# Kernel optimization log

Hardware: AMD Instinct MI355X
Metric: run time of the kernel (lower is better)

The kernel has to match this reference:

```python
import jax, jax.numpy as jnp
import numpy as np

K = 4  # knn_graph(k=4, loop=False) hard-coded in H2GCN.forward


def _knn_2hop_adj(Fet, k):
    """Per-batch kNN graph -> symmetrize -> 2-hop binary adjacency [B,N,N].

    Matches create_adj + get_2hop_neighbors: edge direction and the row
    normalization in create_adj are irrelevant because get_2hop_neighbors
    symmetrizes (adj[row,col]=adj[col,row]=1) and thresholds (adj@adj > 0).
    """
    B, N, _ = Fet.shape
    sq = jnp.sum(Fet * Fet, axis=-1)  # [B,N]
    dist = sq[:, :, None] + sq[:, None, :] - 2.0 * jnp.einsum('bnf,bmf->bnm', Fet, Fet)
    eye = jnp.eye(N, dtype=bool)
    dist = jnp.where(eye[None], jnp.inf, dist)  # loop=False: exclude self
    _, idx = jax.lax.top_k(-dist, k)  # [B,N,k] nearest-neighbor indices
    b_idx = jnp.arange(B)[:, None, None]
    n_idx = jnp.arange(N)[None, :, None]
    A = jnp.zeros((B, N, N), Fet.dtype).at[b_idx, n_idx, idx].set(1.0)
    A = jnp.maximum(A, jnp.swapaxes(A, 1, 2))  # symmetrize 1-hop
    A2 = jnp.einsum('bnm,bmk->bnk', A, A)      # 2-hop counts
    A2 = jnp.where(eye[None], 0.0, A2)          # fill_diagonal_(0)
    return (A2 > 0).astype(Fet.dtype)


def _h2gcn_conv(x, A2, w1, b1, w2, b2):
    """H2GCNConv on dense binary adjacency.

    Dense matmul with binary A2 == gather(x[col]) -> fc2 -> index_add over rows;
    A2.sum(-1) == bincount(row). Degree clamped to >= 1.
    """
    ego = jnp.einsum('bnf,of->bno', x, w1) + b1   # fc1(x)
    msg = jnp.einsum('bnf,of->bno', x, w2) + b2   # fc2(x)
    agg = jnp.einsum('bnm,bmo->bno', A2, msg)     # scatter-add of neighbor msgs
    deg = jnp.maximum(jnp.sum(A2, axis=-1, keepdims=True), 1.0)
    return jax.nn.relu(jnp.concatenate([ego, agg / deg], axis=-1))


def setup_inputs() -> dict:
    key = jax.random.key(0)
    ks = jax.random.split(key, 8)
    B, N, F, NH, NC = 128, 197, 768, 512, 1000
    s = 0.02
    return {
        'Fet': jax.random.normal(ks[0], (B, N, F), jnp.float32),
        'w1_0': jax.random.normal(ks[1], (NH, F), jnp.float32) * s,
        'b1_0': jnp.zeros((NH,), jnp.float32),
        'w2_0': jax.random.normal(ks[2], (NH, F), jnp.float32) * s,
        'b2_0': jnp.zeros((NH,), jnp.float32),
        'w1_1': jax.random.normal(ks[3], (NH, 2 * NH), jnp.float32) * s,
        'b1_1': jnp.zeros((NH,), jnp.float32),
        'w2_1': jax.random.normal(ks[4], (NH, 2 * NH), jnp.float32) * s,
        'b2_1': jnp.zeros((NH,), jnp.float32),
        'fc1_w': jax.random.normal(ks[5], (NH, 4 * NH), jnp.float32) * s,
        'fc1_b': jnp.zeros((NH,), jnp.float32),
        'fc2_w': jax.random.normal(ks[6], (NC, NH), jnp.float32) * s,
        'fc2_b': jnp.zeros((NC,), jnp.float32),
    }


def reference(Fet, w1_0, b1_0, w2_0, b2_0, w1_1, b1_1, w2_1, b2_1,
              fc1_w, fc1_b, fc2_w, fc2_b):
    A2 = _knn_2hop_adj(Fet, K)
    h1 = _h2gcn_conv(Fet, A2, w1_0, b1_0, w2_0, b2_0)   # [B,N,2*nhid]
    h2 = _h2gcn_conv(h1, A2, w1_1, b1_1, w2_1, b2_1)    # [B,N,2*nhid]
    h = jnp.concatenate([h1, h2], axis=-1)              # [B,N,final_dim]
    graph_features = jnp.mean(h, axis=1)                # global_mean_pool
    p = jax.nn.relu(graph_features @ fc1_w.T + fc1_b)   # dropout is identity (eval)
    out = p @ fc2_w.T + fc2_b
    return (out, graph_features)
```

## Files before the change

### kernel.cpp

```cpp
#include <hip/hip_runtime.h>
#include <hip/hip_bf16.h>
#include <math.h>

typedef __attribute__((ext_vector_type(8))) short bf16x8;
typedef __attribute__((ext_vector_type(4))) float f32x4;

#define B_ 128
#define N_ 197
#define F_ 768
#define NH_ 512
#define D2_ 1024
#define D4_ 2048
#define NC_ 1000
#define ROWS_ (B_ * N_)
#define KA_ 224
#define NA_ 256
#define LDG_ 200
#define MT_LD_ (B_ * KA_)

#define OFF_G0     0ull
#define OFF_SQ     20172800ull
#define OFF_ABITS  20273664ull
#define OFF_DEG    21080576ull
#define OFF_FETHI  21181440ull
#define OFF_MSGT   60011520ull
#define OFF_H1     89371648ull
#define OFF_FETLO  OFF_MSGT
#define OFF_POOL   141014016ull
#define OFF_P      142062592ull
#define OFF_WC1    142324736ull
#define OFF_WC2    143897600ull
#define OFF_G1     145994752ull

__device__ __forceinline__ void gll16(const void* g, void* l) {
  __builtin_amdgcn_global_load_lds((const __attribute__((address_space(1))) void*)g,
                                   (__attribute__((address_space(3))) void*)l, 16, 0, 0);
}


__global__ __launch_bounds__(256) void cast_weights(const float* __restrict__ w10,
                                                    const float* __restrict__ w20,
                                                    const float* __restrict__ w11,
                                                    const float* __restrict__ w21,
                                                    __hip_bfloat16* __restrict__ wc1,
                                                    __hip_bfloat16* __restrict__ wc2) {
  const int S1 = NH_ * F_ / 4;
  const int S2 = NH_ * D2_ / 4;
  int i = blockIdx.x * 256 + threadIdx.x;
  const float* src;
  __hip_bfloat16* dst;
  int off;
  if (i < S1) { src = w10; dst = wc1; off = i; }
  else if (i < 2 * S1) { src = w20; dst = wc1 + (size_t)NH_ * F_; off = i - S1; }
  else if (i < 2 * S1 + S2) { src = w11; dst = wc2; off = i - 2 * S1; }
  else { src = w21; dst = wc2 + (size_t)NH_ * D2_; off = i - 2 * S1 - S2; }
  float4 v = ((const float4*)src)[off];
  union { __hip_bfloat16 h[4]; uint2 u; } pk;
  pk.h[0] = __float2bfloat16(v.x);
  pk.h[1] = __float2bfloat16(v.y);
  pk.h[2] = __float2bfloat16(v.z);
  pk.h[3] = __float2bfloat16(v.w);
  ((uint2*)dst)[off] = pk.u;
}

__global__ __launch_bounds__(256) void cast_hilo_sq(const float* __restrict__ X,
                                                    __hip_bfloat16* __restrict__ hi,
                                                    __hip_bfloat16* __restrict__ lo,
                                                    float* __restrict__ sq) {
  int row = blockIdx.x * 4 + (threadIdx.x >> 6);
  int lane = threadIdx.x & 63;
  const float4* xp = (const float4*)(X + (size_t)row * F_);
  uint2* hp = (uint2*)(hi + (size_t)row * F_);
  uint2* lp = (uint2*)(lo + (size_t)row * F_);
  float s = 0.f;
#pragma unroll
  for (int i = 0; i < 3; i++) {
    float4 v = xp[lane + i * 64];
    s += v.x * v.x + v.y * v.y + v.z * v.z + v.w * v.w;
    float f[4] = {v.x, v.y, v.z, v.w};
    union { __hip_bfloat16 h[4]; uint2 u; } ph, pl;
#pragma unroll
    for (int k = 0; k < 4; k++) {
      __hip_bfloat16 h = __float2bfloat16(f[k]);
      ph.h[k] = h;
      pl.h[k] = __float2bfloat16(f[k] - __bfloat162float(h));
    }
    hp[lane + i * 64] = ph.u;
    lp[lane + i * 64] = pl.u;
  }
#pragma unroll
  for (int o = 32; o > 0; o >>= 1) s += __shfl_down(s, o);
  if (lane == 0) sq[row] = s;
}

__global__ __launch_bounds__(256) void mfma_gram(const __hip_bfloat16* __restrict__ Xhi,
                                                 const __hip_bfloat16* __restrict__ Xlo,
                                                 float* __restrict__ g0,
                                                 float* __restrict__ g1) {
  __shared__ short AsH[4096];
  __shared__ short BsH[4096];
  __shared__ short AsL[4096];
  __shared__ short BsL[4096];
  const int t = threadIdx.x;
  const int wgid = blockIdx.x;
  const int L = (wgid & 7) * 96 + (wgid >> 3);
  const int b = L / 6;
  const int rbx = L - b * 6;
  const int bx = rbx % 3;
  const int khalf = rbx / 3;
  const int m0 = (bx == 0) ? 0 : 128;
  const int o0 = (bx == 2) ? 128 : 0;
  const bool mirror = (bx == 1);
  const int l = t & 63, w = t >> 6;
  const int wm = (w >> 1) * 64, wn = (w & 1) * 64;
  const int frow = l & 15, fch = l >> 4;
  const size_t rowbase = (size_t)b * N_;
  const char* AhiB = (const char*)(Xhi + (rowbase + m0) * F_);
  const char* AloB = (const char*)(Xlo + (rowbase + m0) * F_);
  const char* BhiB = (const char*)(Xhi + (rowbase + o0) * F_);
  const char* BloB = (const char*)(Xlo + (rowbase + o0) * F_);
  const int rb = F_ * 2;
  char* AsHB = (char*)AsH;
  char* BsHB = (char*)BsH;
  char* AsLB = (char*)AsL;
  char* BsLB = (char*)BsL;
  float* go = khalf ? g1 : g0;
  f32x4 zero = {0.f, 0.f, 0.f, 0.f};
  f32x4 acc[4][4];
#pragma unroll
  for (int i = 0; i < 4; i++)
#pragma unroll
    for (int j = 0; j < 4; j++) acc[i][j] = zero;
  const int kt0 = khalf * 12;
  for (int kt = kt0; kt < kt0 + 12; kt++) {
    const int kb = kt * 64;
#pragma unroll
    for (int u = 0; u < 2; u++) {
      int prow = u * 32 + (t >> 3);
      int e = (t & 7) ^ (prow & 7);
      int grow = (e >> 2) * 64 + prow;
      size_t goff = (size_t)grow * rb + kb + (e & 3) * 16;
      gll16(AhiB + goff, AsHB + u * 4096 + t * 16);
      gll16(BhiB + goff, BsHB + u * 4096 + t * 16);
      gll16(AloB + goff, AsLB + u * 4096 + t * 16);
      gll16(BloB + goff, BsLB + u * 4096 + t * 16);
    }
    __syncthreads();
    bf16x8 ah[4], al[4], bh[4], bl[4];
#pragma unroll
    for (int i = 0; i < 4; i++) {
      int ar = wm + i * 16 + frow;
      int apr = ar & 63;
      int aoff = apr * 128 + (((((ar >> 6) << 2) | fch) ^ (apr & 7)) * 16);
      ah[i] = *(const bf16x8*)(AsHB + aoff);
      al[i] = *(const bf16x8*)(AsLB + aoff);
      int br = wn + i * 16 + frow;
      int bpr = br & 63;
      int boff = bpr * 128 + (((((br >> 6) << 2) | fch) ^ (bpr & 7)) * 16);
      bh[i] = *(const bf16x8*)(BsHB + boff);
      bl[i] = *(const bf16x8*)(BsLB + boff);
    }
#pragma unroll
    for (int i = 0; i < 4; i++)
#pragma unroll
      for (int j = 0; j < 4; j++) {
        acc[i][j] = __builtin_amdgcn_mfma_f32_16x16x32_bf16(bh[j], ah[i], acc[i][j], 0, 0, 0);
        acc[i][j] = __builtin_amdgcn_mfma_f32_16x16x32_bf16(bl[j], ah[i], acc[i][j], 0, 0, 0);
        acc[i][j] = __builtin_amdgcn_mfma_f32_16x16x32_bf16(bh[j], al[i], acc[i][j], 0, 0, 0);
      }
    __syncthreads();
  }
#pragma unroll
  for (int i = 0; i < 4; i++) {
    int n = m0 + wm + i * 16 + frow;
    if (n >= N_) continue;
    float* gr = go + (rowbase + n) * LDG_;
#pragma unroll
    for (int j = 0; j < 4; j++) {
      int mb = o0 + wn + j * 16 + fch * 4;
      if (mb >= LDG_) continue;
      f32x4 pv = acc[i][j];
      *(f32x4*)&gr[mb] = pv;
      if (mirror) {
#pragma unroll
        for (int r = 0; r < 4; r++)
          go[(rowbase + mb + r) * LDG_ + n] = pv[r];
      }
    }
  }
}

__global__ __launch_bounds__(256) void topk_kernel(const float* __restrict__ g0,
                                                   const float* __restrict__ g1,
                                                   const float* __restrict__ sq,
                                                   unsigned long long* __restrict__ Abits) {
  int row = blockIdx.x * 4 + (threadIdx.x >> 6);
  int lane = threadIdx.x & 63;
  int b = row / N_, n = row - b * N_;
  const float* g0r = g0 + (size_t)row * LDG_;
  const float* g1r = g1 + (size_t)row * LDG_;
  const float* sqb = sq + (size_t)b * N_;
  float v[4];
  int vi[4];
#pragma unroll
  for (int i = 0; i < 4; i++) {
    int m = lane + i * 64;
    bool ok = (m < N_) && (m != n);
    v[i] = ok ? (sqb[m] - 2.f * (g0r[m] + g1r[m])) : INFINITY;
    vi[i] = ok ? m : 0x3fffffff;
  }
  unsigned long long nbr[4] = {0ull, 0ull, 0ull, 0ull};
#pragma unroll
  for (int t = 0; t < 4; t++) {
    float bv = v[0];
    int bi = vi[0];
#pragma unroll
    for (int i = 1; i < 4; i++)
      if (v[i] < bv || (v[i] == bv && vi[i] < bi)) { bv = v[i]; bi = vi[i]; }
#pragma unroll
    for (int o = 1; o < 64; o <<= 1) {
      float ov = __shfl_xor(bv, o);
      int oi = __shfl_xor(bi, o);
      if (ov < bv || (ov == bv && oi < bi)) { bv = ov; bi = oi; }
    }
#pragma unroll
    for (int i = 0; i < 4; i++)
      if (vi[i] == bi) { v[i] = INFINITY; vi[i] = 0x3fffffff; }
    if (lane == 0) {
      nbr[bi >> 6] |= 1ull << (bi & 63);
      atomicOr(&Abits[((size_t)b * N_ + bi) * 4 + (n >> 6)], 1ull << (n & 63));
    }
  }
  if (lane == 0) {
#pragma unroll
    for (int w = 0; w < 4; w++)
      if (nbr[w]) atomicOr(&Abits[(size_t)row * 4 + w], nbr[w]);
  }
}

__global__ __launch_bounds__(256) void a2_kernel(const unsigned long long* __restrict__ Abits,
                                                 __hip_bfloat16* __restrict__ A2bf,
                                                 float* __restrict__ deg) {
  int row = blockIdx.x * 4 + (threadIdx.x >> 6);
  int lane = threadIdx.x & 63;
  int b = row / N_, n = row - b * N_;
  const unsigned long long* arow = Abits + (size_t)row * 4;
  const unsigned long long* base = Abits + (size_t)b * N_ * 4;
  unsigned long long r0 = 0, r1 = 0, r2 = 0, r3 = 0;
#pragma unroll
  for (int w = 0; w < 4; w++) {
    if ((arow[w] >> lane) & 1ull) {
      const unsigned long long* mr = base + (size_t)(w * 64 + lane) * 4;
      r0 |= mr[0]; r1 |= mr[1]; r2 |= mr[2]; r3 |= mr[3];
    }
  }
#pragma unroll
  for (int o = 1; o < 64; o <<= 1) {
    r0 |= __shfl_xor(r0, o);
    r1 |= __shfl_xor(r1, o);
    r2 |= __shfl_xor(r2, o);
    r3 |= __shfl_xor(r3, o);
  }
  unsigned long long rr[4] = {r0, r1, r2, r3};
  rr[n >> 6] &= ~(1ull << (n & 63));
  const int pad = b & 3;
  __hip_bfloat16* out = A2bf + ((size_t)b * NA_ + n) * KA_;
  const __hip_bfloat16 one = __float2bfloat16(1.f);
  const __hip_bfloat16 zer = __float2bfloat16(0.f);
#pragma unroll
  for (int i = 0; i < 4; i++) {
    int m = lane + i * 64;
    if (m < KA_) {
      int k = m - pad;
      bool bit = (k >= 0 && k < N_ && ((rr[k >> 6] >> (k & 63)) & 1ull));
      out[m] = bit ? one : zer;
    }
  }
  if (lane == 0) {
    int dg = __popcll(rr[0]) + __popcll(rr[1]) + __popcll(rr[2]) + __popcll(rr[3]);
    deg[row] = (float)(dg > 0 ? dg : 1);
  }
}

template <int MODE>
__global__ __launch_bounds__(256) void mfma_fused(const __hip_bfloat16* __restrict__ X,
                                                  const __hip_bfloat16* __restrict__ Wcat,
                                                  const float* __restrict__ biasE,
                                                  const float* __restrict__ biasM,
                                                  __hip_bfloat16* __restrict__ h1,
                                                  __hip_bfloat16* __restrict__ msgT,
                                                  float* __restrict__ pool,
                                                  int K) {
  __shared__ short As[4096];
  __shared__ short Bs[4096];
  const int t = threadIdx.x;
  const int wgid = blockIdx.x;
  const int L = (wgid & 7) * 197 + (wgid >> 3);
  const int m0 = (L >> 3) * 128, o0 = (L & 7) * 128;
  const int l = t & 63, w = t >> 6;
  const int wm = (w >> 1) * 64, wn = (w & 1) * 64;
  const int frow = l & 15, fch = l >> 4;
  const char* Abase = (const char*)(X + (size_t)m0 * K);
  const char* Bbase = (const char*)(Wcat + (size_t)o0 * K);
  const int rb = K * 2;
  char* AsB = (char*)As;
  char* BsB = (char*)Bs;
  const bool ego = (o0 < 512);
  const bool swap = (MODE == 1) && ego;
  f32x4 zero = {0.f, 0.f, 0.f, 0.f};
  f32x4 acc[4][4];
#pragma unroll
  for (int i = 0; i < 4; i++)
#pragma unroll
    for (int j = 0; j < 4; j++) acc[i][j] = zero;
  const int KT = K >> 5;
  for (int kt = 0; kt < KT; kt++) {
    const int kb = kt * 64;
#pragma unroll
    for (int u = 0; u < 2; u++) {
      int prow = u * 32 + (t >> 3);
      int e = (t & 7) ^ (prow & 7);
      int grow = (e >> 2) * 64 + prow;
      size_t goff = (size_t)grow * rb + kb + (e & 3) * 16;
      gll16(Abase + goff, AsB + u * 4096 + t * 16);
      gll16(Bbase + goff, BsB + u * 4096 + t * 16);
    }
    __syncthreads();
    bf16x8 af[4], bfv[4];
#pragma unroll
    for (int i = 0; i < 4; i++) {
      int ar = wm + i * 16 + frow;
      int apr = ar & 63;
      af[i] = *(const bf16x8*)(AsB + apr * 128 + (((((ar >> 6) << 2) | fch) ^ (apr & 7)) * 16));
      int br = wn + i * 16 + frow;
      int bpr = br & 63;
      bfv[i] = *(const bf16x8*)(BsB + bpr * 128 + (((((br >> 6) << 2) | fch) ^ (bpr & 7)) * 16));
    }
    if (!swap) {
#pragma unroll
      for (int i = 0; i < 4; i++)
#pragma unroll
        for (int j = 0; j < 4; j++)
          acc[i][j] = __builtin_amdgcn_mfma_f32_16x16x32_bf16(af[i], bfv[j], acc[i][j], 0, 0, 0);
    } else {
#pragma unroll
      for (int i = 0; i < 4; i++)
#pragma unroll
        for (int j = 0; j < 4; j++)
          acc[i][j] = __builtin_amdgcn_mfma_f32_16x16x32_bf16(bfv[j], af[i], acc[i][j], 0, 0, 0);
    }
    __syncthreads();
  }
  if (ego) {
    if (MODE == 1) {
      const int rw = m0 + wm;
      const int b0 = rw / N_;
      const int rloc = (b0 + 1) * N_ - rw;
#pragma unroll
      for (int j = 0; j < 4; j++) {
        int c0 = o0 + wn + j * 16 + fch * 4;
        float4 b4 = *(const float4*)&biasE[c0];
        float bb4[4] = {b4.x, b4.y, b4.z, b4.w};
        float sA4[4] = {0.f, 0.f, 0.f, 0.f};
        float sB4[4] = {0.f, 0.f, 0.f, 0.f};
#pragma unroll
        for (int i = 0; i < 4; i++) {
          int xloc = i * 16 + frow;
          union { __hip_bfloat16 h[4]; uint2 u; } pk;
#pragma unroll
          for (int r = 0; r < 4; r++) {
            float v = fmaxf(acc[i][j][r] + bb4[r], 0.f);
            pk.h[r] = __float2bfloat16(v);
            if (xloc < rloc) sA4[r] += v; else sB4[r] += v;
          }
          *(uint2*)&h1[(size_t)(rw + xloc) * D2_ + c0] = pk.u;
        }
#pragma unroll
        for (int r = 0; r < 4; r++) {
          float sA = sA4[r], sB = sB4[r];
          sA += __shfl_down(sA, 8, 16); sA += __shfl_down(sA, 4, 16);
          sA += __shfl_down(sA, 2, 16); sA += __shfl_down(sA, 1, 16);
          sB += __shfl_down(sB, 8, 16); sB += __shfl_down(sB, 4, 16);
          sB += __shfl_down(sB, 2, 16); sB += __shfl_down(sB, 1, 16);
          if ((l & 15) == 0) {
            atomicAdd(&pool[(size_t)b0 * D4_ + c0 + r], sA);
            if (rloc < 64) atomicAdd(&pool[(size_t)(b0 + 1) * D4_ + c0 + r], sB);
          }
        }
      }
    } else {
#pragma unroll
      for (int j = 0; j < 4; j++) {
        int c = o0 + wn + j * 16 + frow;
        float bv = biasE[c];
        int rw = m0 + wm;
        int b0 = rw / N_;
        int rB = (b0 + 1) * N_;
        float sA = 0.f, sB = 0.f;
#pragma unroll
        for (int i = 0; i < 4; i++) {
          int r0 = m0 + wm + i * 16 + fch * 4;
#pragma unroll
          for (int r = 0; r < 4; r++) {
            float v = fmaxf(acc[i][j][r] + bv, 0.f);
            if (r0 + r < rB) sA += v; else sB += v;
          }
        }
        sA += __shfl_down(sA, 32);
        sA += __shfl_down(sA, 16);
        sB += __shfl_down(sB, 32);
        sB += __shfl_down(sB, 16);
        if (l < 16) {
          atomicAdd(&pool[(size_t)b0 * D4_ + D2_ + c], sA);
          if (rw + 64 > rB) atomicAdd(&pool[(size_t)(b0 + 1) * D4_ + D2_ + c], sB);
        }
      }
    }
  } else {
#pragma unroll
    for (int j = 0; j < 4; j++) {
      int cm = (o0 - 512) + wn + j * 16 + frow;
      float bm = biasM[cm];
      __hip_bfloat16* mrow = msgT + (size_t)cm * MT_LD_;
#pragma unroll
      for (int i = 0; i < 4; i++) {
        int x0 = m0 + wm + i * 16 + fch * 4;
        int b0 = x0 / N_;
        int r0 = x0 - b0 * N_;
        union { __hip_bfloat16 h[4]; uint2 u; } pk;
#pragma unroll
        for (int r = 0; r < 4; r++) pk.h[r] = __float2bfloat16(acc[i][j][r] + bm);
        if (r0 + 3 < N_) {
          *(uint2*)&mrow[b0 * KA_ + (b0 & 3) + r0] = pk.u;
        } else {
#pragma unroll
          for (int r = 0; r < 4; r++) {
            int x = x0 + r;
            int bb = x / N_;
            int rx = x - bb * N_;
            mrow[bb * KA_ + (bb & 3) + rx] = pk.h[r];
          }
        }
      }
    }
  }
}

template <int MODE>
__global__ __launch_bounds__(256) void mfma_agg(const __hip_bfloat16* __restrict__ A2bf,
                                                const __hip_bfloat16* __restrict__ msgT,
                                                const float* __restrict__ deg,
                                                __hip_bfloat16* __restrict__ h1,
                                                float* __restrict__ pool, int poolOff) {
  __shared__ short As[4096];
  __shared__ short Bs[4096];
  const int t = threadIdx.x;
  const int wgid = blockIdx.x;
  const int L = (wgid & 7) * 128 + (wgid >> 3);
  const int b = L >> 3;
  const int o0 = ((L >> 1) & 3) * 128;
  const int m0 = (L & 1) * 128;
  const int l = t & 63, w = t >> 6;
  const int wm = (w >> 1) * 64, wn = (w & 1) * 64;
  const int frow = l & 15, fch = l >> 4;
  const char* Abase = (const char*)(A2bf + ((size_t)b * NA_ + m0) * KA_);
  const char* Bbase = (const char*)(msgT + (size_t)o0 * MT_LD_ + (size_t)b * KA_);
  char* AsB = (char*)As;
  char* BsB = (char*)Bs;
  f32x4 zero = {0.f, 0.f, 0.f, 0.f};
  f32x4 acc[4][4];
#pragma unroll
  for (int i = 0; i < 4; i++)
#pragma unroll
    for (int j = 0; j < 4; j++) acc[i][j] = zero;
  for (int kt = 0; kt < 7; kt++) {
    const int kb = kt * 64;
#pragma unroll
    for (int u = 0; u < 2; u++) {
      int prow = u * 32 + (t >> 3);
      int e = (t & 7) ^ (prow & 7);
      int grow = (e >> 2) * 64 + prow;
      gll16(Abase + (size_t)grow * (KA_ * 2) + kb + (e & 3) * 16, AsB + u * 4096 + t * 16);
      gll16(Bbase + (size_t)grow * (MT_LD_ * 2) + kb + (e & 3) * 16, BsB + u * 4096 + t * 16);
    }
    __syncthreads();
    bf16x8 af[4], bfv[4];
#pragma unroll
    for (int i = 0; i < 4; i++) {
      int ar = wm + i * 16 + frow;
      int apr = ar & 63;
      af[i] = *(const bf16x8*)(AsB + apr * 128 + (((((ar >> 6) << 2) | fch) ^ (apr & 7)) * 16));
      int br = wn + i * 16 + frow;
      int bpr = br & 63;
      bfv[i] = *(const bf16x8*)(BsB + bpr * 128 + (((((br >> 6) << 2) | fch) ^ (bpr & 7)) * 16));
    }
#pragma unroll
    for (int i = 0; i < 4; i++)
#pragma unroll
      for (int j = 0; j < 4; j++)
        acc[i][j] = __builtin_amdgcn_mfma_f32_16x16x32_bf16(bfv[j], af[i], acc[i][j], 0, 0, 0);
    __syncthreads();
  }
  float sv[4][4];
#pragma unroll
  for (int j = 0; j < 4; j++)
#pragma unroll
    for (int r = 0; r < 4; r++) sv[j][r] = 0.f;
#pragma unroll
  for (int i = 0; i < 4; i++) {
    int n = m0 + wm + i * 16 + frow;
    bool ok = (n < N_);
    float dinv = ok ? (1.f / deg[b * N_ + n]) : 0.f;
#pragma unroll
    for (int j = 0; j < 4; j++) {
      int c0 = o0 + wn + j * 16 + fch * 4;
      union { __hip_bfloat16 h[4]; uint2 u; } pk;
#pragma unroll
      for (int r = 0; r < 4; r++) {
        float v = ok ? fmaxf(acc[i][j][r] * dinv, 0.f) : 0.f;
        sv[j][r] += v;
        pk.h[r] = __float2bfloat16(v);
      }
      if (MODE == 0 && ok)
        *(uint2*)&h1[((size_t)b * N_ + n) * D2_ + NH_ + c0] = pk.u;
    }
  }
#pragma unroll
  for (int j = 0; j < 4; j++) {
#pragma unroll
    for (int r = 0; r < 4; r++) {
      float s = sv[j][r];
      s += __shfl_down(s, 8, 16);
      s += __shfl_down(s, 4, 16);
      s += __shfl_down(s, 2, 16);
      s += __shfl_down(s, 1, 16);
      if ((l & 15) == 0)
        atomicAdd(&pool[(size_t)b * D4_ + poolOff + o0 + wn + j * 16 + fch * 4 + r], s);
    }
  }
}

__global__ __launch_bounds__(256) void scale_pool(const float* __restrict__ pool,
                                                  float* __restrict__ gf) {
  int b = blockIdx.y;
  int c = blockIdx.x * 256 + threadIdx.x;
  gf[(size_t)b * D4_ + c] = pool[(size_t)b * D4_ + c] * (1.f / N_);
}

template <bool RELUX>
__global__ __launch_bounds__(256) void head_gemm(const float* __restrict__ Xg,
                                                 const float* __restrict__ W,
                                                 const float* __restrict__ bias,
                                                 float* __restrict__ Y,
                                                 int Rows, int Fin, int O, int kchunk) {
  __shared__ float Xs[16][68];
  __shared__ float Ws[16][68];
  int tx = threadIdx.x, ty = threadIdx.y;
  int tid = ty * 16 + tx;
  int lr = tid >> 2;
  int lk = (tid & 3) * 4;
  int rbase = blockIdx.y * 64;
  int o0 = blockIdx.x * 64;
  int k0base = blockIdx.z * kchunk;
  float acc[4][4] = {};
  for (int k0 = k0base; k0 < k0base + kchunk; k0 += 16) {
    float4 xv = make_float4(0.f, 0.f, 0.f, 0.f);
    if (rbase + lr < Rows) xv = *(const float4*)&Xg[(size_t)(rbase + lr) * Fin + k0 + lk];
    if (RELUX) {
      xv.x = fmaxf(xv.x, 0.f); xv.y = fmaxf(xv.y, 0.f);
      xv.z = fmaxf(xv.z, 0.f); xv.w = fmaxf(xv.w, 0.f);
    }
    Xs[lk][lr] = xv.x; Xs[lk + 1][lr] = xv.y; Xs[lk + 2][lr] = xv.z; Xs[lk + 3][lr] = xv.w;
    float4 wv = make_float4(0.f, 0.f, 0.f, 0.f);
    if (o0 + lr < O) wv = *(const float4*)&W[(size_t)(o0 + lr) * Fin + k0 + lk];
    Ws[lk][lr] = wv.x; Ws[lk + 1][lr] = wv.y; Ws[lk + 2][lr] = wv.z; Ws[lk + 3][lr] = wv.w;
    __syncthreads();
#pragma unroll
    for (int k = 0; k < 16; k++) {
      float4 a = *(const float4*)&Xs[k][ty * 4];
      float4 bb = *(const float4*)&Ws[k][tx * 4];
      float av[4] = {a.x, a.y, a.z, a.w};
      float bv[4] = {bb.x, bb.y, bb.z, bb.w};
#pragma unroll
      for (int i = 0; i < 4; i++)
#pragma unroll
        for (int j = 0; j < 4; j++) acc[i][j] = fmaf(av[i], bv[j], acc[i][j]);
    }
    __syncthreads();
  }
#pragma unroll
  for (int i = 0; i < 4; i++) {
    int rrow = rbase + ty * 4 + i;
    if (rrow >= Rows) continue;
#pragma unroll
    for (int j = 0; j < 4; j++) {
      int c = o0 + tx * 4 + j;
      if (c >= O) continue;
      float vv = acc[i][j] + ((blockIdx.z == 0) ? bias[c] : 0.f);
      atomicAdd(&Y[(size_t)rrow * O + c], vv);
    }
  }
}

extern "C" void kernel_launch(void* const* d_in, const int* in_sizes, int n_in,
                              void* d_out, int out_size, void* d_ws, size_t ws_size,
                              hipStream_t stream) {
  const float* Fet  = (const float*)d_in[0];
  const float* w1_0 = (const float*)d_in[1];
  const float* b1_0 = (const float*)d_in[2];
  const float* w2_0 = (const float*)d_in[3];
  const float* b2_0 = (const float*)d_in[4];
  const float* w1_1 = (const float*)d_in[5];
  const float* b1_1 = (const float*)d_in[6];
  const float* w2_1 = (const float*)d_in[7];
  const float* b2_1 = (const float*)d_in[8];
  const float* fc1_w = (const float*)d_in[9];
  const float* fc1_b = (const float*)d_in[10];
  const float* fc2_w = (const float*)d_in[11];
  const float* fc2_b = (const float*)d_in[12];

  char* ws = (char*)d_ws;
  float* g0 = (float*)(ws + OFF_G0);
  float* g1 = (float*)(ws + OFF_G1);
  __hip_bfloat16* A2bf = (__hip_bfloat16*)(ws + OFF_G0);
  float* sq = (float*)(ws + OFF_SQ);
  unsigned long long* Abits = (unsigned long long*)(ws + OFF_ABITS);
  float* deg = (float*)(ws + OFF_DEG);
  __hip_bfloat16* Fet_hi = (__hip_bfloat16*)(ws + OFF_FETHI);
  __hip_bfloat16* Fet_lo = (__hip_bfloat16*)(ws + OFF_FETLO);
  __hip_bfloat16* msgT = (__hip_bfloat16*)(ws + OFF_MSGT);
  __hip_bfloat16* h1 = (__hip_bfloat16*)(ws + OFF_H1);
  float* pool = (float*)(ws + OFF_POOL);
  float* p = (float*)(ws + OFF_P);
  __hip_bfloat16* wc1 = (__hip_bfloat16*)(ws + OFF_WC1);
  __hip_bfloat16* wc2 = (__hip_bfloat16*)(ws + OFF_WC2);

  float* out = (float*)d_out;
  float* gf = out + (size_t)B_ * NC_;

  hipMemsetAsync(Abits, 0, (size_t)ROWS_ * 4 * sizeof(unsigned long long), stream);
  hipMemsetAsync(pool, 0, (size_t)B_ * D4_ * sizeof(float), stream);
  hipMemsetAsync(p, 0, (size_t)B_ * NH_ * sizeof(float), stream);
  hipMemsetAsync(out, 0, (size_t)B_ * NC_ * sizeof(float), stream);

  cast_hilo_sq<<<ROWS_ / 4, 256, 0, stream>>>(Fet, Fet_hi, Fet_lo, sq);
  cast_weights<<<1792, 256, 0, stream>>>(w1_0, w2_0, w1_1, w2_1, wc1, wc2);

  mfma_gram<<<768, 256, 0, stream>>>(Fet_hi, Fet_lo, g0, g1);
  topk_kernel<<<ROWS_ / 4, 256, 0, stream>>>(g0, g1, sq, Abits);
  a2_kernel<<<ROWS_ / 4, 256, 0, stream>>>(Abits, A2bf, deg);

  mfma_fused<1><<<1576, 256, 0, stream>>>(Fet_hi, wc1, b1_0, b2_0, h1, msgT, pool, F_);
  mfma_agg<0><<<1024, 256, 0, stream>>>(A2bf, msgT, deg, h1, pool, NH_);

  mfma_fused<2><<<1576, 256, 0, stream>>>(h1, wc2, b1_1, b2_1, nullptr, msgT, pool, D2_);
  mfma_agg<1><<<1024, 256, 0, stream>>>(A2bf, msgT, deg, nullptr, pool, D2_ + NH_);

  scale_pool<<<dim3(8, B_), 256, 0, stream>>>(pool, gf);

  head_gemm<false><<<dim3(8, 2, 16), dim3(16, 16), 0, stream>>>(
      gf, fc1_w, fc1_b, p, B_, D4_, NH_, 128);
  head_gemm<true><<<dim3(16, 2, 8), dim3(16, 16), 0, stream>>>(
      p, fc2_w, fc2_b, out, B_, NH_, NC_, 64);
}
```

Measured before the change: 444.6 us.

## Double-buffer LDS tiles in the fused and aggregation MFMA GEMM kernels

Both bf16 MFMA GEMM kernels now keep two LDS buffers for the A and B tiles. Each iteration issues the global-to-LDS loads for the next k-tile before doing the fragment reads and MFMAs on the current one, so memory latency can overlap compute instead of stalling behind a barrier. The stage address offsets are hoisted out of the loop. In exchange, LDS use per workgroup doubles, which may lower occupancy, and overlap only lasts until the barrier that closes each iteration.

```diff
diff --git a/kernel.cpp b/kernel.cpp
--- a/kernel.cpp
+++ b/kernel.cpp
@@ -291,8 +291,8 @@
                                                   __hip_bfloat16* __restrict__ msgT,
                                                   float* __restrict__ pool,
                                                   int K) {
-  __shared__ short As[4096];
-  __shared__ short Bs[4096];
+  __shared__ short As[2][4096];
+  __shared__ short Bs[2][4096];
   const int t = threadIdx.x;
   const int wgid = blockIdx.x;
   const int L = (wgid & 7) * 197 + (wgid >> 3);
@@ -307,6 +307,18 @@
   char* BsB = (char*)Bs;
   const bool ego = (o0 < 512);
   const bool swap = (MODE == 1) && ego;
+  const int sp = t >> 3;
+  const int se = (t & 7) ^ (sp & 7);
+  const size_t goff0 = (size_t)((se >> 2) * 64 + sp) * rb + (se & 3) * 16;
+  const size_t goff1 = (size_t)((se >> 2) * 64 + 32 + sp) * rb + (se & 3) * 16;
+  auto stage = [&](int buf, int kt) {
+    const int kb = kt * 64;
+    const int d = buf * 8192 + t * 16;
+    gll16(Abase + goff0 + kb, AsB + d);
+    gll16(Abase + goff1 + kb, AsB + d + 4096);
+    gll16(Bbase + goff0 + kb, BsB + d);
+    gll16(Bbase + goff1 + kb, BsB + d + 4096);
+  };
   f32x4 zero = {0.f, 0.f, 0.f, 0.f};
   f32x4 acc[4][4];
 #pragma unroll
@@ -314,27 +326,22 @@
 #pragma unroll
     for (int j = 0; j < 4; j++) acc[i][j] = zero;
   const int KT = K >> 5;
+  stage(0, 0);
+  __syncthreads();
   for (int kt = 0; kt < KT; kt++) {
-    const int kb = kt * 64;
-#pragma unroll
-    for (int u = 0; u < 2; u++) {
-      int prow = u * 32 + (t >> 3);
-      int e = (t & 7) ^ (prow & 7);
-      int grow = (e >> 2) * 64 + prow;
-      size_t goff = (size_t)grow * rb + kb + (e & 3) * 16;
-      gll16(Abase + goff, AsB + u * 4096 + t * 16);
-      gll16(Bbase + goff, BsB + u * 4096 + t * 16);
-    }
-    __syncthreads();
+    const int cur = kt & 1;
+    if (kt + 1 < KT) stage(cur ^ 1, kt + 1);
     bf16x8 af[4], bfv[4];
 #pragma unroll
     for (int i = 0; i < 4; i++) {
       int ar = wm + i * 16 + frow;
       int apr = ar & 63;
-      af[i] = *(const bf16x8*)(AsB + apr * 128 + (((((ar >> 6) << 2) | fch) ^ (apr & 7)) * 16));
+      af[i] = *(const bf16x8*)(AsB + cur * 8192 + apr * 128 +
+                               (((((ar >> 6) << 2) | fch) ^ (apr & 7)) * 16));
       int br = wn + i * 16 + frow;
       int bpr = br & 63;
-      bfv[i] = *(const bf16x8*)(BsB + bpr * 128 + (((((br >> 6) << 2) | fch) ^ (bpr & 7)) * 16));
+      bfv[i] = *(const bf16x8*)(BsB + cur * 8192 + bpr * 128 +
+                                (((((br >> 6) << 2) | fch) ^ (bpr & 7)) * 16));
     }
     if (!swap) {
 #pragma unroll
@@ -452,8 +459,8 @@
                                                 const float* __restrict__ deg,
                                                 __hip_bfloat16* __restrict__ h1,
                                                 float* __restrict__ pool, int poolOff) {
-  __shared__ short As[4096];
-  __shared__ short Bs[4096];
+  __shared__ short As[2][4096];
+  __shared__ short Bs[2][4096];
   const int t = threadIdx.x;
   const int wgid = blockIdx.x;
   const int L = (wgid & 7) * 128 + (wgid >> 3);
@@ -467,32 +474,41 @@
   const char* Bbase = (const char*)(msgT + (size_t)o0 * MT_LD_ + (size_t)b * KA_);
   char* AsB = (char*)As;
   char* BsB = (char*)Bs;
+  const int sp = t >> 3;
+  const int se = (t & 7) ^ (sp & 7);
+  const int sg0 = (se >> 2) * 64 + sp;
+  const int sg1 = sg0 + 32;
+  const int sx = (se & 3) * 16;
+  auto stage = [&](int buf, int kt) {
+    const int kb = kt * 64;
+    const int d = buf * 8192 + t * 16;
+    gll16(Abase + (size_t)sg0 * (KA_ * 2) + kb + sx, AsB + d);
+    gll16(Abase + (size_t)sg1 * (KA_ * 2) + kb + sx, AsB + d + 4096);
+    gll16(Bbase + (size_t)sg0 * (MT_LD_ * 2) + kb + sx, BsB + d);
+    gll16(Bbase + (size_t)sg1 * (MT_LD_ * 2) + kb + sx, BsB + d + 4096);
+  };
   f32x4 zero = {0.f, 0.f, 0.f, 0.f};
   f32x4 acc[4][4];
 #pragma unroll
   for (int i = 0; i < 4; i++)
 #pragma unroll
     for (int j = 0; j < 4; j++) acc[i][j] = zero;
+  stage(0, 0);
+  __syncthreads();
   for (int kt = 0; kt < 7; kt++) {
-    const int kb = kt * 64;
-#pragma unroll
-    for (int u = 0; u < 2; u++) {
-      int prow = u * 32 + (t >> 3);
-      int e = (t & 7) ^ (prow & 7);
-      int grow = (e >> 2) * 64 + prow;
-      gll16(Abase + (size_t)grow * (KA_ * 2) + kb + (e & 3) * 16, AsB + u * 4096 + t * 16);
-      gll16(Bbase + (size_t)grow * (MT_LD_ * 2) + kb + (e & 3) * 16, BsB + u * 4096 + t * 16);
-    }
-    __syncthreads();
+    const int cur = kt & 1;
+    if (kt + 1 < 7) stage(cur ^ 1, kt + 1);
     bf16x8 af[4], bfv[4];
 #pragma unroll
     for (int i = 0; i < 4; i++) {
       int ar = wm + i * 16 + frow;
       int apr = ar & 63;
-      af[i] = *(const bf16x8*)(AsB + apr * 128 + (((((ar >> 6) << 2) | fch) ^ (apr & 7)) * 16));
+      af[i] = *(const bf16x8*)(AsB + cur * 8192 + apr * 128 +
+                               (((((ar >> 6) << 2) | fch) ^ (apr & 7)) * 16));
       int br = wn + i * 16 + frow;
       int bpr = br & 63;
-      bfv[i] = *(const bf16x8*)(BsB + bpr * 128 + (((((br >> 6) << 2) | fch) ^ (bpr & 7)) * 16));
+      bfv[i] = *(const bf16x8*)(BsB + cur * 8192 + bpr * 128 +
+                                (((((br >> 6) << 2) | fch) ^ (bpr & 7)) * 16));
     }
 #pragma unroll
     for (int i = 0; i < 4; i++)
```

Result: no change. 440.7 us, median of 3 (-0.9%).

## Load MFMA fragments directly from global memory instead of staging through LDS

Applied to the files above, without the earlier changes.

Both the fused projection GEMM and the aggregation GEMM drop their LDS tiles and barriers, and each wave reads its bf16 fragments straight from global memory. This removes the shared-memory round trip and the __syncthreads stalls per K step. In exchange, tiles are no longer shared across the waves of a workgroup, so global/L2 traffic roughly doubles and there is no explicit prefetch to hide load latency.

```diff
diff --git a/kernel.cpp b/kernel.cpp
--- a/kernel.cpp
+++ b/kernel.cpp
@@ -36,7 +36,6 @@
   __builtin_amdgcn_global_load_lds((const __attribute__((address_space(1))) void*)g,
                                    (__attribute__((address_space(3))) void*)l, 16, 0, 0);
 }
-
 
 __global__ __launch_bounds__(256) void cast_weights(const float* __restrict__ w10,
                                                     const float* __restrict__ w20,
@@ -291,8 +290,6 @@
                                                   __hip_bfloat16* __restrict__ msgT,
                                                   float* __restrict__ pool,
                                                   int K) {
-  __shared__ short As[4096];
-  __shared__ short Bs[4096];
   const int t = threadIdx.x;
   const int wgid = blockIdx.x;
   const int L = (wgid & 7) * 197 + (wgid >> 3);
@@ -300,13 +297,12 @@
   const int l = t & 63, w = t >> 6;
   const int wm = (w >> 1) * 64, wn = (w & 1) * 64;
   const int frow = l & 15, fch = l >> 4;
-  const char* Abase = (const char*)(X + (size_t)m0 * K);
-  const char* Bbase = (const char*)(Wcat + (size_t)o0 * K);
   const int rb = K * 2;
-  char* AsB = (char*)As;
-  char* BsB = (char*)Bs;
   const bool ego = (o0 < 512);
   const bool swap = (MODE == 1) && ego;
+  const char* Ap = (const char*)X + (size_t)(m0 + wm + frow) * rb + fch * 16;
+  const char* Bp = (const char*)Wcat + (size_t)(o0 + wn + frow) * rb + fch * 16;
+  const size_t rstep = (size_t)16 * rb;
   f32x4 zero = {0.f, 0.f, 0.f, 0.f};
   f32x4 acc[4][4];
 #pragma unroll
@@ -315,27 +311,12 @@
     for (int j = 0; j < 4; j++) acc[i][j] = zero;
   const int KT = K >> 5;
   for (int kt = 0; kt < KT; kt++) {
-    const int kb = kt * 64;
-#pragma unroll
-    for (int u = 0; u < 2; u++) {
-      int prow = u * 32 + (t >> 3);
-      int e = (t & 7) ^ (prow & 7);
-      int grow = (e >> 2) * 64 + prow;
-      size_t goff = (size_t)grow * rb + kb + (e & 3) * 16;
-      gll16(Abase + goff, AsB + u * 4096 + t * 16);
-      gll16(Bbase + goff, BsB + u * 4096 + t * 16);
-    }
-    __syncthreads();
+    const size_t kb = (size_t)kt * 64;
     bf16x8 af[4], bfv[4];
 #pragma unroll
-    for (int i = 0; i < 4; i++) {
-      int ar = wm + i * 16 + frow;
-      int apr = ar & 63;
-      af[i] = *(const bf16x8*)(AsB + apr * 128 + (((((ar >> 6) << 2) | fch) ^ (apr & 7)) * 16));
-      int br = wn + i * 16 + frow;
-      int bpr = br & 63;
-      bfv[i] = *(const bf16x8*)(BsB + bpr * 128 + (((((br >> 6) << 2) | fch) ^ (bpr & 7)) * 16));
-    }
+    for (int i = 0; i < 4; i++) af[i] = *(const bf16x8*)(Ap + i * rstep + kb);
+#pragma unroll
+    for (int j = 0; j < 4; j++) bfv[j] = *(const bf16x8*)(Bp + j * rstep + kb);
     if (!swap) {
 #pragma unroll
       for (int i = 0; i < 4; i++)
@@ -349,7 +330,6 @@
         for (int j = 0; j < 4; j++)
           acc[i][j] = __builtin_amdgcn_mfma_f32_16x16x32_bf16(bfv[j], af[i], acc[i][j], 0, 0, 0);
     }
-    __syncthreads();
   }
   if (ego) {
     if (MODE == 1) {
@@ -452,8 +432,6 @@
                                                 const float* __restrict__ deg,
                                                 __hip_bfloat16* __restrict__ h1,
                                                 float* __restrict__ pool, int poolOff) {
-  __shared__ short As[4096];
-  __shared__ short Bs[4096];
   const int t = threadIdx.x;
   const int wgid = blockIdx.x;
   const int L = (wgid & 7) * 128 + (wgid >> 3);
@@ -463,10 +441,10 @@
   const int l = t & 63, w = t >> 6;
   const int wm = (w >> 1) * 64, wn = (w & 1) * 64;
   const int frow = l & 15, fch = l >> 4;
-  const char* Abase = (const char*)(A2bf + ((size_t)b * NA_ + m0) * KA_);
-  const char* Bbase = (const char*)(msgT + (size_t)o0 * MT_LD_ + (size_t)b * KA_);
-  char* AsB = (char*)As;
-  char* BsB = (char*)Bs;
+  const char* Ap = (const char*)(A2bf + ((size_t)b * NA_ + m0 + wm + frow) * KA_) + fch * 16;
+  const char* Bp = (const char*)(msgT + (size_t)(o0 + wn + frow) * MT_LD_ + (size_t)b * KA_) + fch * 16;
+  const size_t rstepA = (size_t)16 * KA_ * 2;
+  const size_t rstepB = (size_t)16 * MT_LD_ * 2;
   f32x4 zero = {0.f, 0.f, 0.f, 0.f};
   f32x4 acc[4][4];
 #pragma unroll
@@ -474,32 +452,17 @@
 #pragma unroll
     for (int j = 0; j < 4; j++) acc[i][j] = zero;
   for (int kt = 0; kt < 7; kt++) {
-    const int kb = kt * 64;
-#pragma unroll
-    for (int u = 0; u < 2; u++) {
-      int prow = u * 32 + (t >> 3);
-      int e = (t & 7) ^ (prow & 7);
-      int grow = (e >> 2) * 64 + prow;
-      gll16(Abase + (size_t)grow * (KA_ * 2) + kb + (e & 3) * 16, AsB + u * 4096 + t * 16);
-      gll16(Bbase + (size_t)grow * (MT_LD_ * 2) + kb + (e & 3) * 16, BsB + u * 4096 + t * 16);
-    }
-    __syncthreads();
+    const size_t kb = (size_t)kt * 64;
     bf16x8 af[4], bfv[4];
 #pragma unroll
-    for (int i = 0; i < 4; i++) {
-      int ar = wm + i * 16 + frow;
-      int apr = ar & 63;
-      af[i] = *(const bf16x8*)(AsB + apr * 128 + (((((ar >> 6) << 2) | fch) ^ (apr & 7)) * 16));
-      int br = wn + i * 16 + frow;
-      int bpr = br & 63;
-      bfv[i] = *(const bf16x8*)(BsB + bpr * 128 + (((((br >> 6) << 2) | fch) ^ (bpr & 7)) * 16));
-    }
+    for (int i = 0; i < 4; i++) af[i] = *(const bf16x8*)(Ap + i * rstepA + kb);
+#pragma unroll
+    for (int j = 0; j < 4; j++) bfv[j] = *(const bf16x8*)(Bp + j * rstepB + kb);
 #pragma unroll
     for (int i = 0; i < 4; i++)
 #pragma unroll
       for (int j = 0; j < 4; j++)
         acc[i][j] = __builtin_amdgcn_mfma_f32_16x16x32_bf16(bfv[j], af[i], acc[i][j], 0, 0, 0);
-    __syncthreads();
   }
   float sv[4][4];
 #pragma unroll
```

Result: slower. 637.4 us (+43.4%).
